# Optimization experiments

Measured on AMD Instinct MI355X. Metric: run time of the kernel, lower is better.

The kernel has to match this reference:

```python
import jax, jax.numpy as jnp
import numpy as np

B, LD, D, CONV = 2048, 100, 128, 128
C = CONV * 4  # 512
KS = (4, 6, 8)  # drug conv kernels -> Ld = 100 - 15 = 85


def setup_inputs() -> dict:
    key = jax.random.key(0)
    ks = jax.random.split(key, 32)
    def w(k, shape):
        return jax.random.normal(k, shape, jnp.float32) * 0.05
    emb = w(ks[0], (65, D)).at[0].set(0.0)  # padding_idx=0
    return dict(
        drug=jax.random.randint(ks[1], (B, LD), 0, 65, jnp.int32),
        feature=jax.random.normal(ks[2], (B, 7), jnp.float32),
        emb=emb,
        dw1=w(ks[3], (CONV, D, KS[0])), db1=w(ks[4], (CONV,)),
        dw2=w(ks[5], (CONV * 2, CONV, KS[1])), db2=w(ks[6], (CONV * 2,)),
        dw3=w(ks[7], (C, CONV * 2, KS[2])), db3=w(ks[8], (C,)),
        fw1=w(ks[9], (CONV, 7, 3)), fb1=w(ks[10], (CONV,)),
        fw2=w(ks[11], (CONV * 2, CONV, 3)), fb2=w(ks[12], (CONV * 2,)),
        fw3=w(ks[13], (C, CONV * 2, 3)), fb3=w(ks[14], (C,)),
        Wda=w(ks[15], (C, C)), bda=w(ks[16], (C,)),
        Wfa=w(ks[17], (C, C)), bfa=w(ks[18], (C,)),
        Watt=w(ks[19], (C, C)), batt=w(ks[20], (C,)),
        W1=w(ks[21], (1024, 2 * C)), b1=w(ks[22], (1024,)),
        W2=w(ks[23], (1024, 1024)), b2=w(ks[24], (1024,)),
        W3=w(ks[25], (512, 1024)), b3=w(ks[26], (512,)),
        Wo=w(ks[27], (1, 512)), bo=w(ks[28], (1,)),
    )


def _conv1d(x, w, b, pad):
    # x: [B, Cin, L], w: [Cout, Cin, K] (torch layout)
    y = jax.lax.conv_general_dilated(x, w, (1,), [(pad, pad)],
                                     dimension_numbers=('NCH', 'OIH', 'NCH'))
    return y + b[None, :, None]


def reference(drug, feature, emb, dw1, db1, dw2, db2, dw3, db3,
              fw1, fb1, fw2, fb2, fw3, fb3,
              Wda, bda, Wfa, bfa, Watt, batt,
              W1, b1, W2, b2, W3, b3, Wo, bo):
    relu = jax.nn.relu
    # Drug CNN stack (valid convs)
    x = emb[drug].transpose(0, 2, 1)                    # [B, D, 100]
    h = relu(_conv1d(x, dw1, db1, 0))
    h = relu(_conv1d(h, dw2, db2, 0))
    drugConv = relu(_conv1d(h, dw3, db3, 0))            # [B, C, 85]
    drug_att = jnp.einsum('bcl,dc->bld', drugConv, Wda) + bda   # [B, 85, C]
    # Feature CNN stack (same-padded convs on length-1 sequence)
    f = feature.reshape(feature.shape[0], 7, -1)        # [B, 7, 1]
    h = relu(_conv1d(f, fw1, fb1, 1))
    h = relu(_conv1d(h, fw2, fb2, 1))
    featureNN = relu(_conv1d(h, fw3, fb3, 1))           # [B, C, 1]
    feature_att = jnp.einsum('bcl,dc->bld', featureNN, Wfa) + bfa  # [B, 1, C]
    # Broadcast outer-sum cross attention
    s = relu(drug_att[:, :, None, :] + feature_att[:, None, :, :])  # [B,85,1,C]
    A = jnp.einsum('bqfc,dc->bqfd', s, Watt) + batt
    comp = jax.nn.sigmoid(jnp.mean(A, axis=2).transpose(0, 2, 1))   # [B,C,85]
    feat = jax.nn.sigmoid(jnp.mean(A, axis=1).transpose(0, 2, 1))   # [B,C,1]
    drugConv = drugConv * (0.5 + comp)
    featureNN = featureNN * (0.5 + feat)
    vd = jnp.max(drugConv, axis=2)                      # global max pool, kernel == Ld
    vf = featureNN[:, :, 0]                             # squeeze(2), Lf == 1
    pair = jnp.concatenate([vd, vf], axis=1)            # [B, 2C]
    leaky = lambda z: jnp.where(z > 0, z, 0.01 * z)
    h1 = leaky(pair @ W1.T + b1)
    h2 = leaky(h1 @ W2.T + b2)
    h3 = leaky(h2 @ W3.T + b3)
    return h3 @ Wo.T + bo                               # [B, 1]
```

## Files before the change

### kernel.cpp

```cpp
#include <hip/hip_runtime.h>
#include <cstdint>
#include <cstddef>

typedef unsigned short ushort_t;
typedef __bf16 bf16x8 __attribute__((ext_vector_type(8)));
typedef float floatx4 __attribute__((ext_vector_type(4)));

#define DEV static __device__ __forceinline__

DEV ushort_t f2bf(float f){
  union { float f; uint32_t u; } v; v.f = f;
  uint32_t u = v.u;
  return (ushort_t)((u + 0x7fffu + ((u >> 16) & 1u)) >> 16);
}
DEV float bf2f(ushort_t h){
  union { uint32_t u; float f; } v; v.u = ((uint32_t)h) << 16; return v.f;
}
DEV float sigmoidf_(float x){ return 1.f / (1.f + __expf(-x)); }

#define AS1 __attribute__((address_space(1)))
#define AS3 __attribute__((address_space(3)))
DEV void gld_lds16(const void* g, void* l){
  __builtin_amdgcn_global_load_lds((const AS1 void*)g, (AS3 void*)l, 16, 0, 0);
}

DEV void swz_xy(int& nx, int& my){
  int gx = gridDim.x, gy = gridDim.y;
  int lin = blockIdx.x + gx * blockIdx.y;
  int full = gy & ~7;
  int region = full * gx;
  if (lin < region){ int q = lin >> 3; nx = q % gx; my = (q / gx) * 8 + (lin & 7); }
  else { int r = lin - region; nx = r % gx; my = full + r / gx; }
}

#define BN 2048
#define LD 100
#define DIM 128
#define L1 97
#define L2 92
#define L3 85
#define CC 512

struct PrepArgs {
  const float *dw1,*dw2,*dw3,*Wda,*Wfa,*Watt,*W1,*W2,*W3,*fw1,*fw2,*fw3;
  ushort_t *bt1,*bt2,*bt3,*bWda,*bWfa,*bWatt,*bW1,*bW2,*bW3;
  float *fw1m,*fw2m,*fw3m;
};

__global__ void prep_k(PrepArgs a){
  int t0 = blockIdx.x * blockDim.x + threadIdx.x;
  int stride = gridDim.x * blockDim.x;
  switch (blockIdx.y){
  case 0:
    for (int i=t0;i<128*512;i+=stride){ int o=i>>9, rem=i&511, kk=rem>>7, c=rem&127;
      a.bt1[i]=f2bf(a.dw1[o*512 + c*4 + kk]); } break;
  case 1:
    for (int i=t0;i<256*768;i+=stride){ int o=i/768, rem=i-o*768, kk=rem>>7, c=rem&127;
      a.bt2[i]=f2bf(a.dw2[o*768 + c*6 + kk]); } break;
  case 2:
    for (int i=t0;i<512*2048;i+=stride){ int o=i>>11, rem=i&2047, kk=rem>>8, c=rem&255;
      a.bt3[i]=f2bf(a.dw3[o*2048 + c*8 + kk]); } break;
  case 3: for (int i=t0;i<262144;i+=stride) a.bWda[i]=f2bf(a.Wda[i]); break;
  case 4: for (int i=t0;i<262144;i+=stride) a.bWfa[i]=f2bf(a.Wfa[i]); break;
  case 5: for (int i=t0;i<262144;i+=stride) a.bWatt[i]=f2bf(a.Watt[i]); break;
  case 6: for (int i=t0;i<1048576;i+=stride) a.bW1[i]=f2bf(a.W1[i]); break;
  case 7: for (int i=t0;i<1048576;i+=stride) a.bW2[i]=f2bf(a.W2[i]); break;
  case 8: for (int i=t0;i<524288;i+=stride) a.bW3[i]=f2bf(a.W3[i]); break;
  case 9:  for (int i=t0;i<7*128;i+=stride){ int ii=i>>7, o=i&127; a.fw1m[i]=a.fw1[o*21 + ii*3 + 1]; } break;
  case 10: for (int i=t0;i<128*256;i+=stride){ int ii=i>>8, o=i&255; a.fw2m[i]=a.fw2[o*384 + ii*3 + 1]; } break;
  case 11: for (int i=t0;i<256*512;i+=stride){ int ii=i>>9, o=i&511; a.fw3m[i]=a.fw3[o*768 + ii*3 + 1]; } break;
  }
}

__global__ void gather_k(const int* __restrict__ drug, const float* __restrict__ emb,
                         ushort_t* __restrict__ x, int total){
  int g = blockIdx.x * blockDim.x + threadIdx.x;
  if (g >= total) return;
  int c8 = g & 15; int t = g >> 4;
  int tok = drug[t];
  const float* src = emb + (size_t)tok*DIM + c8*8;
  ushort_t* dst = x + ((size_t)t*DIM + c8*8);
  #pragma unroll
  for (int k=0;k<8;k++) dst[k] = f2bf(src[k]);
}

__global__ void featnn_k(const float* __restrict__ feature,
                         const float* __restrict__ fw1m, const float* __restrict__ fb1,
                         const float* __restrict__ fw2m, const float* __restrict__ fb2,
                         const float* __restrict__ fw3m, const float* __restrict__ fb3,
                         float* __restrict__ fnnf, ushort_t* __restrict__ fnnb)
{
  __shared__ float fs[8][7];
  __shared__ float h1s[8][128];
  __shared__ float h2s[8][256];
  int b0 = blockIdx.x * 8;
  int tid = threadIdx.x;
  if (tid < 56){ int bb = tid/7, i = tid - bb*7; fs[bb][i] = feature[(b0+bb)*7 + i]; }
  __syncthreads();
  if (tid < 128){
    float acc[8]; float bias = fb1[tid];
    #pragma unroll
    for (int bb=0;bb<8;bb++) acc[bb]=bias;
    for (int i=0;i<7;i++){ float wv = fw1m[i*128+tid];
      #pragma unroll
      for (int bb=0;bb<8;bb++) acc[bb] += wv*fs[bb][i]; }
    #pragma unroll
    for (int bb=0;bb<8;bb++) h1s[bb][tid]=fmaxf(acc[bb],0.f);
  }
  __syncthreads();
  {
    float acc[8]; float bias = fb2[tid];
    #pragma unroll
    for (int bb=0;bb<8;bb++) acc[bb]=bias;
    for (int i=0;i<128;i++){ float wv = fw2m[i*256+tid];
      #pragma unroll
      for (int bb=0;bb<8;bb++) acc[bb] += wv*h1s[bb][i]; }
    #pragma unroll
    for (int bb=0;bb<8;bb++) h2s[bb][tid]=fmaxf(acc[bb],0.f);
  }
  __syncthreads();
  #pragma unroll
  for (int oo=0;oo<2;oo++){
    int o = tid + oo*256;
    float acc[8]; float bias = fb3[o];
    #pragma unroll
    for (int bb=0;bb<8;bb++) acc[bb]=bias;
    for (int i=0;i<256;i++){ float wv = fw3m[i*512+o];
      #pragma unroll
      for (int bb=0;bb<8;bb++) acc[bb] += wv*h2s[bb][i]; }
    #pragma unroll
    for (int bb=0;bb<8;bb++){
      float v = fmaxf(acc[bb],0.f);
      fnnf[(size_t)(b0+bb)*CC + o] = v;
      fnnb[(size_t)(b0+bb)*CC + o] = f2bf(v);
    }
  }
}

enum { EP_RELU_BIAS=0, EP_RELU_BIAS_FATT=1, EP_ATT=2, EP_LEAKY_BIAS=3, EP_BIAS_F32=4 };

template<int EP>
__global__ __launch_bounds__(256,3) void gemm_k(
    const ushort_t* __restrict__ A, const ushort_t* __restrict__ Bt,
    int K, int LoutA, int LinA, int CinA,
    const float* __restrict__ bias, const float* __restrict__ fatt,
    void* __restrict__ outp, int ldo,
    const ushort_t* __restrict__ dcp, float* __restrict__ asum_g, float* __restrict__ tmax_g)
{
  __shared__ __align__(16) ushort_t As[128*64];
  __shared__ __align__(16) ushort_t Bs[128*64];
  const int tid  = threadIdx.x;
  const int lane = tid & 63;
  const int w    = tid >> 6;
  int nx, my; swz_xy(nx, my);
  const int m0 = my * 128;
  const int n0 = nx * 128;
  const int chunk = (lane & 7) ^ (lane >> 3);

  const ushort_t* pa[4];
  const ushort_t* pb[4];
  #pragma unroll
  for (int it=0; it<4; ++it){
    int row = it*32 + w*8 + (lane>>3);
    int r = m0 + row;
    int bb = r / LoutA;
    int ll = r - bb*LoutA;
    pa[it] = A  + ((size_t)(bb*LinA + ll) * (size_t)CinA + (size_t)chunk*8);
    pb[it] = Bt + ((size_t)(n0+row) * (size_t)K + (size_t)chunk*8);
  }

  floatx4 acc[4][4];
  #pragma unroll
  for (int i=0;i<4;i++)
    #pragma unroll
    for (int j=0;j<4;j++) acc[i][j] = (floatx4){0.f,0.f,0.f,0.f};

  const int mw = (w & 1) * 64;
  const int nw = (w >> 1) * 64;

  for (int k0=0; k0<K; k0+=64){
    #pragma unroll
    for (int it=0; it<4; ++it){
      gld_lds16(pa[it], &As[(it*32 + w*8)*64]);
      gld_lds16(pb[it], &Bs[(it*32 + w*8)*64]);
      pa[it] += 64; pb[it] += 64;
    }
    __syncthreads();
    #pragma unroll
    for (int ks=0; ks<2; ++ks){
      bf16x8 af[4], bfr[4];
      #pragma unroll
      for (int i=0;i<4;i++){
        int rowa = mw + i*16 + (lane & 15);
        int rowb = nw + i*16 + (lane & 15);
        int j = ks*4 + (lane >> 4);
        af[i]  = *(const bf16x8*)&As[rowa*64 + ((j ^ (rowa & 7)) << 3)];
        bfr[i] = *(const bf16x8*)&Bs[rowb*64 + ((j ^ (rowb & 7)) << 3)];
      }
      #pragma unroll
      for (int i=0;i<4;i++)
        #pragma unroll
        for (int j=0;j<4;j++)
          acc[i][j] = __builtin_amdgcn_mfma_f32_16x16x32_bf16(af[i], bfr[j], acc[i][j], 0, 0, 0);
    }
    __syncthreads();
  }

  if constexpr (EP == EP_ATT){
    __shared__ float red_sum[3*128];
    __shared__ int   red_max[3*128];
    const int bfirst = m0 / L3;
    for (int t2 = tid; t2 < 3*128; t2 += 256){ red_sum[t2] = 0.f; red_max[t2] = 0; }
    __syncthreads();
    const int segA = (m0 + mw) / L3 - bfirst;
    #pragma unroll
    for (int j=0;j<4;j++){
      int col = nw + j*16 + (lane & 15);
      int n = n0 + col;
      float bi = bias[n];
      float s0 = 0.f, s1 = 0.f, x0 = 0.f, x1 = 0.f;
      #pragma unroll
      for (int i=0;i<4;i++){
        #pragma unroll
        for (int r4=0;r4<4;r4++){
          int m = m0 + mw + i*16 + (lane>>4)*4 + r4;
          float Av = acc[i][j][r4] + bi;
          float dcv = bf2f(dcp[(size_t)m*CC + n]);
          float tv = dcv * (0.5f + sigmoidf_(Av));
          if ((m / L3 - bfirst) == segA){ s0 += Av; x0 = fmaxf(x0, tv); }
          else                          { s1 += Av; x1 = fmaxf(x1, tv); }
        }
      }
      atomicAdd(&red_sum[segA*128 + col], s0);
      atomicMax(&red_max[segA*128 + col], __float_as_int(x0));
      if (segA + 1 < 3){
        atomicAdd(&red_sum[(segA+1)*128 + col], s1);
        atomicMax(&red_max[(segA+1)*128 + col], __float_as_int(x1));
      }
    }
    __syncthreads();
    for (int t2 = tid; t2 < 3*128; t2 += 256){
      int seg = t2 >> 7, col = t2 & 127;
      int b = bfirst + seg;
      if (b * L3 < m0 + 128){
        atomicAdd(asum_g + (size_t)b*CC + n0 + col, red_sum[t2]);
        atomicMax((int*)tmax_g + (size_t)b*CC + n0 + col, red_max[t2]);
      }
    }
    return;
  }

  float* outf = (float*)outp;
  ushort_t* outh = (ushort_t*)outp;
  #pragma unroll
  for (int i=0;i<4;i++){
    #pragma unroll
    for (int j=0;j<4;j++){
      #pragma unroll
      for (int r4=0;r4<4;r4++){
        int m = m0 + mw + i*16 + (lane>>4)*4 + r4;
        int n = n0 + nw + j*16 + (lane & 15);
        float v = acc[i][j][r4] + bias[n];
        if constexpr (EP == EP_RELU_BIAS)       v = fmaxf(v, 0.f);
        else if constexpr (EP == EP_RELU_BIAS_FATT){ v += fatt[(m / L3)*CC + n]; v = fmaxf(v, 0.f); }
        else if constexpr (EP == EP_LEAKY_BIAS) v = v > 0.f ? v : 0.01f*v;
        if constexpr (EP == EP_BIAS_F32) outf[(size_t)m*ldo + n] = v;
        else                             outh[(size_t)m*ldo + n] = f2bf(v);
      }
    }
  }
}

__global__ void reduce2_k(const float* __restrict__ asum, const float* __restrict__ tmax,
                          const float* __restrict__ fnnf, ushort_t* __restrict__ pair)
{
  int g = blockIdx.x * blockDim.x + threadIdx.x;
  if (g >= BN * CC) return;
  int b = g >> 9, c = g & 511;
  pair[(size_t)b*1024 + c] = f2bf(tmax[g]);
  float fv = fnnf[g] * (0.5f + sigmoidf_(asum[g] * (1.f/(float)L3)));
  pair[(size_t)b*1024 + 512 + c] = f2bf(fv);
}

__global__ void final_k(const ushort_t* __restrict__ h3, const float* __restrict__ Wo,
                        const float* __restrict__ bo, float* __restrict__ out)
{
  int b = blockIdx.x*4 + (threadIdx.x >> 6);
  int lane = threadIdx.x & 63;
  float acc = 0.f;
  for (int i=lane; i<512; i+=64) acc += bf2f(h3[(size_t)b*512 + i]) * Wo[i];
  #pragma unroll
  for (int off=32; off; off>>=1) acc += __shfl_down(acc, off);
  if (lane == 0) out[b] = acc + bo[0];
}

extern "C" void kernel_launch(void* const* d_in, const int* in_sizes, int n_in,
                              void* d_out, int out_size, void* d_ws, size_t ws_size,
                              hipStream_t stream)
{
  (void)in_sizes; (void)n_in; (void)out_size;
  const int*   drug    = (const int*)  d_in[0];
  const float* feature = (const float*)d_in[1];
  const float* emb     = (const float*)d_in[2];
  const float* dw1 = (const float*)d_in[3];  const float* db1 = (const float*)d_in[4];
  const float* dw2 = (const float*)d_in[5];  const float* db2 = (const float*)d_in[6];
  const float* dw3 = (const float*)d_in[7];  const float* db3 = (const float*)d_in[8];
  const float* fw1 = (const float*)d_in[9];  const float* fb1 = (const float*)d_in[10];
  const float* fw2 = (const float*)d_in[11]; const float* fb2 = (const float*)d_in[12];
  const float* fw3 = (const float*)d_in[13]; const float* fb3 = (const float*)d_in[14];
  const float* Wda = (const float*)d_in[15]; const float* bda = (const float*)d_in[16];
  const float* Wfa = (const float*)d_in[17]; const float* bfa = (const float*)d_in[18];
  const float* Watt= (const float*)d_in[19]; const float* batt= (const float*)d_in[20];
  const float* W1  = (const float*)d_in[21]; const float* b1  = (const float*)d_in[22];
  const float* W2  = (const float*)d_in[23]; const float* b2  = (const float*)d_in[24];
  const float* W3  = (const float*)d_in[25]; const float* b3  = (const float*)d_in[26];
  const float* Wo  = (const float*)d_in[27]; const float* bo  = (const float*)d_in[28];
  float* out = (float*)d_out;

  size_t off = 0; char* base = (char*)d_ws;
  auto alloc = [&](size_t bytes)->char*{
    off = (off + 255) & ~(size_t)255; char* p = base + off; off += bytes; return p;
  };
  ushort_t* bt1  = (ushort_t*)alloc(128*512*2);
  ushort_t* bt2  = (ushort_t*)alloc(256*768*2);
  ushort_t* bt3  = (ushort_t*)alloc((size_t)512*2048*2);
  ushort_t* bWda = (ushort_t*)alloc(262144*2);
  ushort_t* bWfa = (ushort_t*)alloc(262144*2);
  ushort_t* bWatt= (ushort_t*)alloc(262144*2);
  ushort_t* bW1  = (ushort_t*)alloc((size_t)1048576*2);
  ushort_t* bW2  = (ushort_t*)alloc((size_t)1048576*2);
  ushort_t* bW3  = (ushort_t*)alloc((size_t)524288*2);
  float* fw1m = (float*)alloc(7*128*4);
  float* fw2m = (float*)alloc(128*256*4);
  float* fw3m = (float*)alloc(256*512*4);
  float* fnnf = (float*)alloc((size_t)BN*CC*4);
  ushort_t* fnnb = (ushort_t*)alloc((size_t)BN*CC*2);
  float* fattf = (float*)alloc((size_t)BN*CC*4);
  float* asum_g = (float*)alloc((size_t)BN*CC*4);
  float* tmax_g = (float*)alloc((size_t)BN*CC*4);
  ushort_t* pairb = (ushort_t*)alloc((size_t)BN*1024*2);
  ushort_t* m1b = (ushort_t*)alloc((size_t)BN*1024*2);
  ushort_t* m2b = (ushort_t*)alloc((size_t)BN*1024*2);
  ushort_t* m3b = (ushort_t*)alloc((size_t)BN*512*2);

  const size_t PER_SLABP = 97536, PER_DC = 87040, PER_CHUNK = 271616;
  size_t avail = (ws_size > off + 4096) ? (ws_size - off - 4096) : 0;
  int CH = (int)(avail / PER_CHUNK);
  if (CH > BN) CH = BN;
  CH = (CH / 128) * 128;
  if (CH < 128) CH = 128;
  char* chunkbase = alloc((size_t)CH*PER_CHUNK);
  ushort_t* xembC = (ushort_t*)chunkbase;
  ushort_t* h1C   = (ushort_t*)(chunkbase + (size_t)CH*25600);
  ushort_t* h2C   = (ushort_t*)(chunkbase + (size_t)CH*(25600+24832));
  ushort_t* dcC   = (ushort_t*)(chunkbase + (size_t)CH*PER_SLABP);
  ushort_t* sC    = (ushort_t*)(chunkbase + (size_t)CH*(PER_SLABP + PER_DC));

  PrepArgs pa;
  pa.dw1=dw1; pa.dw2=dw2; pa.dw3=dw3; pa.Wda=Wda; pa.Wfa=Wfa; pa.Watt=Watt;
  pa.W1=W1; pa.W2=W2; pa.W3=W3; pa.fw1=fw1; pa.fw2=fw2; pa.fw3=fw3;
  pa.bt1=bt1; pa.bt2=bt2; pa.bt3=bt3; pa.bWda=bWda; pa.bWfa=bWfa; pa.bWatt=bWatt;
  pa.bW1=bW1; pa.bW2=bW2; pa.bW3=bW3; pa.fw1m=fw1m; pa.fw2m=fw2m; pa.fw3m=fw3m;

  hipMemsetAsync(asum_g, 0, (size_t)BN*CC*4, stream);
  hipMemsetAsync(tmax_g, 0, (size_t)BN*CC*4, stream);
  prep_k<<<dim3(64,12), 256, 0, stream>>>(pa);
  featnn_k<<<BN/8, 256, 0, stream>>>(feature, fw1m, fb1, fw2m, fb2, fw3m, fb3, fnnf, fnnb);
  gemm_k<EP_BIAS_F32><<<dim3(4,16), 256, 0, stream>>>(fnnb, bWfa, 512, 1,1,512, bfa, nullptr, fattf, 512, nullptr,nullptr,nullptr);

  for (int b0c = 0; b0c < BN; b0c += CH){
    const int c = (BN - b0c < CH) ? (BN - b0c) : CH;
    const int t = c / 128;
    gather_k<<<(c*LD*(DIM/8) + 255)/256, 256, 0, stream>>>(drug + (size_t)b0c*LD, emb, xembC, c*LD*(DIM/8));
    gemm_k<EP_RELU_BIAS><<<dim3(1, t*L1), 256, 0, stream>>>(xembC, bt1, 512,  L1, LD, DIM, db1, nullptr, h1C, 128, nullptr,nullptr,nullptr);
    gemm_k<EP_RELU_BIAS><<<dim3(2, t*L2), 256, 0, stream>>>(h1C,  bt2, 768,  L2, L1, 128, db2, nullptr, h2C, 256, nullptr,nullptr,nullptr);
    gemm_k<EP_RELU_BIAS><<<dim3(4, t*L3), 256, 0, stream>>>(h2C,  bt3, 2048, L3, L2, 256, db3, nullptr, dcC,  512, nullptr,nullptr,nullptr);
    gemm_k<EP_RELU_BIAS_FATT><<<dim3(4, t*L3), 256, 0, stream>>>(dcC, bWda, 512, 1,1,512, bda, fattf + (size_t)b0c*CC, sC, 512, nullptr,nullptr,nullptr);
    gemm_k<EP_ATT><<<dim3(4, t*L3), 256, 0, stream>>>(sC, bWatt, 512, 1,1,512, batt, nullptr, nullptr, 512,
                                                      dcC, asum_g + (size_t)b0c*CC, tmax_g + (size_t)b0c*CC);
  }

  reduce2_k<<<(BN*CC + 255)/256, 256, 0, stream>>>(asum_g, tmax_g, fnnf, pairb);

  gemm_k<EP_LEAKY_BIAS><<<dim3(8,16), 256, 0, stream>>>(pairb, bW1, 1024, 1,1,1024, b1, nullptr, m1b, 1024, nullptr,nullptr,nullptr);
  gemm_k<EP_LEAKY_BIAS><<<dim3(8,16), 256, 0, stream>>>(m1b,  bW2, 1024, 1,1,1024, b2, nullptr, m2b, 1024, nullptr,nullptr,nullptr);
  gemm_k<EP_LEAKY_BIAS><<<dim3(4,16), 256, 0, stream>>>(m2b,  bW3, 1024, 1,1,1024, b3, nullptr, m3b, 512, nullptr,nullptr,nullptr);
  final_k<<<BN/4, 256, 0, stream>>>(m3b, Wo, bo, out);
}
```

Before: 1.079 ms.

## Fuse drug-attention and attention GEMMs into one kernel keeping s in LDS

Replaces the two back-to-back GEMMs (drugConv@Wda with fatt/ReLU, then s@Watt with the sigmoid/mean/max epilogue) with a single att_k kernel. Each block handles 64 rows, computes s in two 256-column halves directly into swizzled LDS, and accumulates the second GEMM's output in registers across both halves. This removes the global write and read-back of the s intermediate and one launch, and shrinks the per-chunk workspace so larger chunks fit. In exchange the kernel holds many more accumulator registers (launch bounds 2), uses 64-row tiles with repeated Wda/Watt reloads per block, and has no software pipelining, which may lower MFMA efficiency.

```diff
diff --git a/kernel.cpp b/kernel.cpp
--- a/kernel.cpp
+++ b/kernel.cpp
@@ -137,15 +137,14 @@
   }
 }
 
-enum { EP_RELU_BIAS=0, EP_RELU_BIAS_FATT=1, EP_ATT=2, EP_LEAKY_BIAS=3, EP_BIAS_F32=4 };
+enum { EP_RELU_BIAS=0, EP_RELU_BIAS_FATT=1, EP_LEAKY_BIAS=3, EP_BIAS_F32=4 };
 
 template<int EP>
 __global__ __launch_bounds__(256,3) void gemm_k(
     const ushort_t* __restrict__ A, const ushort_t* __restrict__ Bt,
     int K, int LoutA, int LinA, int CinA,
     const float* __restrict__ bias, const float* __restrict__ fatt,
-    void* __restrict__ outp, int ldo,
-    const ushort_t* __restrict__ dcp, float* __restrict__ asum_g, float* __restrict__ tmax_g)
+    void* __restrict__ outp, int ldo)
 {
   __shared__ __align__(16) ushort_t As[128*64];
   __shared__ __align__(16) ushort_t Bs[128*64];
@@ -206,50 +205,6 @@
     __syncthreads();
   }
 
-  if constexpr (EP == EP_ATT){
-    __shared__ float red_sum[3*128];
-    __shared__ int   red_max[3*128];
-    const int bfirst = m0 / L3;
-    for (int t2 = tid; t2 < 3*128; t2 += 256){ red_sum[t2] = 0.f; red_max[t2] = 0; }
-    __syncthreads();
-    const int segA = (m0 + mw) / L3 - bfirst;
-    #pragma unroll
-    for (int j=0;j<4;j++){
-      int col = nw + j*16 + (lane & 15);
-      int n = n0 + col;
-      float bi = bias[n];
-      float s0 = 0.f, s1 = 0.f, x0 = 0.f, x1 = 0.f;
-      #pragma unroll
-      for (int i=0;i<4;i++){
-        #pragma unroll
-        for (int r4=0;r4<4;r4++){
-          int m = m0 + mw + i*16 + (lane>>4)*4 + r4;
-          float Av = acc[i][j][r4] + bi;
-          float dcv = bf2f(dcp[(size_t)m*CC + n]);
-          float tv = dcv * (0.5f + sigmoidf_(Av));
-          if ((m / L3 - bfirst) == segA){ s0 += Av; x0 = fmaxf(x0, tv); }
-          else                          { s1 += Av; x1 = fmaxf(x1, tv); }
-        }
-      }
-      atomicAdd(&red_sum[segA*128 + col], s0);
-      atomicMax(&red_max[segA*128 + col], __float_as_int(x0));
-      if (segA + 1 < 3){
-        atomicAdd(&red_sum[(segA+1)*128 + col], s1);
-        atomicMax(&red_max[(segA+1)*128 + col], __float_as_int(x1));
-      }
-    }
-    __syncthreads();
-    for (int t2 = tid; t2 < 3*128; t2 += 256){
-      int seg = t2 >> 7, col = t2 & 127;
-      int b = bfirst + seg;
-      if (b * L3 < m0 + 128){
-        atomicAdd(asum_g + (size_t)b*CC + n0 + col, red_sum[t2]);
-        atomicMax((int*)tmax_g + (size_t)b*CC + n0 + col, red_max[t2]);
-      }
-    }
-    return;
-  }
-
   float* outf = (float*)outp;
   ushort_t* outh = (ushort_t*)outp;
   #pragma unroll
@@ -267,6 +222,180 @@
         if constexpr (EP == EP_BIAS_F32) outf[(size_t)m*ldo + n] = v;
         else                             outh[(size_t)m*ldo + n] = f2bf(v);
       }
+    }
+  }
+}
+
+__global__ __launch_bounds__(256,2) void att_k(
+    const ushort_t* __restrict__ dcp,
+    const ushort_t* __restrict__ bWda,
+    const float* __restrict__ bda,
+    const float* __restrict__ fatt,
+    const ushort_t* __restrict__ bWatt,
+    const float* __restrict__ batt,
+    float* __restrict__ asum_g, float* __restrict__ tmax_g)
+{
+  __shared__ __align__(16) ushort_t Sh[64*256];
+  __shared__ __align__(16) ushort_t Bs[128*64];
+  __shared__ __align__(16) ushort_t AsR[64*64];
+  float* red_sum = (float*)AsR;
+  int*   red_max = (int*)AsR + 1024;
+
+  const int tid  = threadIdx.x;
+  const int lane = tid & 63;
+  const int w    = tid >> 6;
+  const int m0   = blockIdx.x * 64;
+  const int mh   = (w & 1) * 32;
+  const int nh   = (w >> 1) * 64;
+  const int chunkb = (lane & 7) ^ (lane >> 3);
+
+  const ushort_t* paBase[2];
+  #pragma unroll
+  for (int it=0; it<2; ++it)
+    paBase[it] = dcp + (size_t)(m0 + it*32 + w*8 + (lane>>3))*CC + (size_t)chunkb*8;
+
+  floatx4 acc2[4][2][4];
+  #pragma unroll
+  for (int a=0;a<4;a++)
+    #pragma unroll
+    for (int i=0;i<2;i++)
+      #pragma unroll
+      for (int j=0;j<4;j++) acc2[a][i][j] = (floatx4){0.f,0.f,0.f,0.f};
+
+  for (int h=0; h<2; ++h){
+    #pragma unroll
+    for (int nt=0; nt<2; ++nt){
+      floatx4 acc[2][4];
+      #pragma unroll
+      for (int i=0;i<2;i++)
+        #pragma unroll
+        for (int j=0;j<4;j++) acc[i][j] = (floatx4){0.f,0.f,0.f,0.f};
+      const ushort_t* pa[2] = { paBase[0], paBase[1] };
+      const ushort_t* pb[4];
+      #pragma unroll
+      for (int it=0; it<4; ++it)
+        pb[it] = bWda + (size_t)(h*256 + nt*128 + it*32 + w*8 + (lane>>3))*CC + (size_t)chunkb*8;
+
+      for (int k0=0; k0<512; k0+=64){
+        #pragma unroll
+        for (int it=0; it<2; ++it){ gld_lds16(pa[it], &AsR[(it*32 + w*8)*64]); pa[it] += 64; }
+        #pragma unroll
+        for (int it=0; it<4; ++it){ gld_lds16(pb[it], &Bs[(it*32 + w*8)*64]);  pb[it] += 64; }
+        __syncthreads();
+        #pragma unroll
+        for (int ks=0; ks<2; ++ks){
+          bf16x8 af[2], bfr[4];
+          int j = ks*4 + (lane >> 4);
+          #pragma unroll
+          for (int i=0;i<2;i++){
+            int rowa = mh + i*16 + (lane & 15);
+            af[i] = *(const bf16x8*)&AsR[rowa*64 + ((j ^ (rowa & 7)) << 3)];
+          }
+          #pragma unroll
+          for (int j2=0;j2<4;j2++){
+            int rowb = nh + j2*16 + (lane & 15);
+            bfr[j2] = *(const bf16x8*)&Bs[rowb*64 + ((j ^ (rowb & 7)) << 3)];
+          }
+          #pragma unroll
+          for (int i=0;i<2;i++)
+            #pragma unroll
+            for (int j2=0;j2<4;j2++)
+              acc[i][j2] = __builtin_amdgcn_mfma_f32_16x16x32_bf16(af[i], bfr[j2], acc[i][j2], 0, 0, 0);
+        }
+        __syncthreads();
+      }
+      #pragma unroll
+      for (int i=0;i<2;i++){
+        #pragma unroll
+        for (int j2=0;j2<4;j2++){
+          #pragma unroll
+          for (int r4=0;r4<4;r4++){
+            int row = mh + i*16 + (lane>>4)*4 + r4;
+            int cl  = nt*128 + nh + j2*16 + (lane & 15);
+            int gn  = h*256 + cl;
+            float v = acc[i][j2][r4] + bda[gn] + fatt[(size_t)((m0+row)/L3)*CC + gn];
+            v = fmaxf(v, 0.f);
+            Sh[row*256 + ((((cl>>3) ^ (row & 7)) << 3) | (cl & 7))] = f2bf(v);
+          }
+        }
+      }
+    }
+    __syncthreads();
+
+    #pragma unroll
+    for (int nt2=0; nt2<4; ++nt2){
+      const ushort_t* pb[4];
+      #pragma unroll
+      for (int it=0; it<4; ++it)
+        pb[it] = bWatt + (size_t)(nt2*128 + it*32 + w*8 + (lane>>3))*CC + h*256 + (size_t)chunkb*8;
+      for (int k0=0; k0<256; k0+=64){
+        #pragma unroll
+        for (int it=0; it<4; ++it){ gld_lds16(pb[it], &Bs[(it*32 + w*8)*64]); pb[it] += 64; }
+        __syncthreads();
+        #pragma unroll
+        for (int ks=0; ks<2; ++ks){
+          bf16x8 af[2], bfr[4];
+          int j = ks*4 + (lane >> 4);
+          int cj = (k0 >> 3) + j;
+          #pragma unroll
+          for (int i=0;i<2;i++){
+            int row = mh + i*16 + (lane & 15);
+            af[i] = *(const bf16x8*)&Sh[row*256 + ((cj ^ (row & 7)) << 3)];
+          }
+          #pragma unroll
+          for (int j2=0;j2<4;j2++){
+            int rowb = nh + j2*16 + (lane & 15);
+            bfr[j2] = *(const bf16x8*)&Bs[rowb*64 + ((j ^ (rowb & 7)) << 3)];
+          }
+          #pragma unroll
+          for (int i=0;i<2;i++)
+            #pragma unroll
+            for (int j2=0;j2<4;j2++)
+              acc2[nt2][i][j2] = __builtin_amdgcn_mfma_f32_16x16x32_bf16(af[i], bfr[j2], acc2[nt2][i][j2], 0, 0, 0);
+        }
+        __syncthreads();
+      }
+    }
+  }
+
+  for (int t2 = tid; t2 < 1024; t2 += 256){ red_sum[t2] = 0.f; red_max[t2] = 0; }
+  __syncthreads();
+  const int bfirst = m0 / L3;
+  const int segW = (m0 + mh) / L3 - bfirst;
+  #pragma unroll
+  for (int nt2=0; nt2<4; ++nt2){
+    #pragma unroll
+    for (int j2=0;j2<4;j2++){
+      int n = nt2*128 + nh + j2*16 + (lane & 15);
+      float s0=0.f, s1=0.f, x0=0.f, x1=0.f;
+      float bi = batt[n];
+      #pragma unroll
+      for (int i=0;i<2;i++){
+        #pragma unroll
+        for (int r4=0;r4<4;r4++){
+          int m = m0 + mh + i*16 + (lane>>4)*4 + r4;
+          float Av = acc2[nt2][i][j2][r4] + bi;
+          float dcv = bf2f(dcp[(size_t)m*CC + n]);
+          float tv = dcv * (0.5f + sigmoidf_(Av));
+          if (m / L3 - bfirst == segW){ s0 += Av; x0 = fmaxf(x0, tv); }
+          else                        { s1 += Av; x1 = fmaxf(x1, tv); }
+        }
+      }
+      atomicAdd(&red_sum[segW*512 + n], s0);
+      atomicMax(&red_max[segW*512 + n], __float_as_int(x0));
+      if (segW == 0){
+        atomicAdd(&red_sum[512 + n], s1);
+        atomicMax(&red_max[512 + n], __float_as_int(x1));
+      }
+    }
+  }
+  __syncthreads();
+  for (int t2 = tid; t2 < 1024; t2 += 256){
+    int seg = t2 >> 9, col = t2 & 511;
+    int b = bfirst + seg;
+    if (b*L3 < m0 + 64 && b*L3 + L3 > m0){
+      atomicAdd(asum_g + (size_t)b*CC + col, red_sum[t2]);
+      atomicMax((int*)tmax_g + (size_t)b*CC + col, red_max[t2]);
     }
   }
 }
@@ -343,7 +472,7 @@
   ushort_t* m2b = (ushort_t*)alloc((size_t)BN*1024*2);
   ushort_t* m3b = (ushort_t*)alloc((size_t)BN*512*2);
 
-  const size_t PER_SLABP = 97536, PER_DC = 87040, PER_CHUNK = 271616;
+  const size_t PER_SLABP = 97536, PER_DC = 87040, PER_CHUNK = PER_SLABP + PER_DC;
   size_t avail = (ws_size > off + 4096) ? (ws_size - off - 4096) : 0;
   int CH = (int)(avail / PER_CHUNK);
   if (CH > BN) CH = BN;
@@ -354,7 +483,6 @@
   ushort_t* h1C   = (ushort_t*)(chunkbase + (size_t)CH*25600);
   ushort_t* h2C   = (ushort_t*)(chunkbase + (size_t)CH*(25600+24832));
   ushort_t* dcC   = (ushort_t*)(chunkbase + (size_t)CH*PER_SLABP);
-  ushort_t* sC    = (ushort_t*)(chunkbase + (size_t)CH*(PER_SLABP + PER_DC));
 
   PrepArgs pa;
   pa.dw1=dw1; pa.dw2=dw2; pa.dw3=dw3; pa.Wda=Wda; pa.Wfa=Wfa; pa.Watt=Watt;
@@ -366,24 +494,23 @@
   hipMemsetAsync(tmax_g, 0, (size_t)BN*CC*4, stream);
   prep_k<<<dim3(64,12), 256, 0, stream>>>(pa);
   featnn_k<<<BN/8, 256, 0, stream>>>(feature, fw1m, fb1, fw2m, fb2, fw3m, fb3, fnnf, fnnb);
-  gemm_k<EP_BIAS_F32><<<dim3(4,16), 256, 0, stream>>>(fnnb, bWfa, 512, 1,1,512, bfa, nullptr, fattf, 512, nullptr,nullptr,nullptr);
+  gemm_k<EP_BIAS_F32><<<dim3(4,16), 256, 0, stream>>>(fnnb, bWfa, 512, 1,1,512, bfa, nullptr, fattf, 512);
 
   for (int b0c = 0; b0c < BN; b0c += CH){
     const int c = (BN - b0c < CH) ? (BN - b0c) : CH;
     const int t = c / 128;
     gather_k<<<(c*LD*(DIM/8) + 255)/256, 256, 0, stream>>>(drug + (size_t)b0c*LD, emb, xembC, c*LD*(DIM/8));
-    gemm_k<EP_RELU_BIAS><<<dim3(1, t*L1), 256, 0, stream>>>(xembC, bt1, 512,  L1, LD, DIM, db1, nullptr, h1C, 128, nullptr,nullptr,nullptr);
-    gemm_k<EP_RELU_BIAS><<<dim3(2, t*L2), 256, 0, stream>>>(h1C,  bt2, 768,  L2, L1, 128, db2, nullptr, h2C, 256, nullptr,nullptr,nullptr);
-    gemm_k<EP_RELU_BIAS><<<dim3(4, t*L3), 256, 0, stream>>>(h2C,  bt3, 2048, L3, L2, 256, db3, nullptr, dcC,  512, nullptr,nullptr,nullptr);
-    gemm_k<EP_RELU_BIAS_FATT><<<dim3(4, t*L3), 256, 0, stream>>>(dcC, bWda, 512, 1,1,512, bda, fattf + (size_t)b0c*CC, sC, 512, nullptr,nullptr,nullptr);
-    gemm_k<EP_ATT><<<dim3(4, t*L3), 256, 0, stream>>>(sC, bWatt, 512, 1,1,512, batt, nullptr, nullptr, 512,
-                                                      dcC, asum_g + (size_t)b0c*CC, tmax_g + (size_t)b0c*CC);
+    gemm_k<EP_RELU_BIAS><<<dim3(1, t*L1), 256, 0, stream>>>(xembC, bt1, 512,  L1, LD, DIM, db1, nullptr, h1C, 128);
+    gemm_k<EP_RELU_BIAS><<<dim3(2, t*L2), 256, 0, stream>>>(h1C,  bt2, 768,  L2, L1, 128, db2, nullptr, h2C, 256);
+    gemm_k<EP_RELU_BIAS><<<dim3(4, t*L3), 256, 0, stream>>>(h2C,  bt3, 2048, L3, L2, 256, db3, nullptr, dcC,  512);
+    att_k<<<dim3(t*170), 256, 0, stream>>>(dcC, bWda, bda, fattf + (size_t)b0c*CC, bWatt, batt,
+                                           asum_g + (size_t)b0c*CC, tmax_g + (size_t)b0c*CC);
   }
 
   reduce2_k<<<(BN*CC + 255)/256, 256, 0, stream>>>(asum_g, tmax_g, fnnf, pairb);
 
-  gemm_k<EP_LEAKY_BIAS><<<dim3(8,16), 256, 0, stream>>>(pairb, bW1, 1024, 1,1,1024, b1, nullptr, m1b, 1024, nullptr,nullptr,nullptr);
-  gemm_k<EP_LEAKY_BIAS><<<dim3(8,16), 256, 0, stream>>>(m1b,  bW2, 1024, 1,1,1024, b2, nullptr, m2b, 1024, nullptr,nullptr,nullptr);
-  gemm_k<EP_LEAKY_BIAS><<<dim3(4,16), 256, 0, stream>>>(m2b,  bW3, 1024, 1,1,1024, b3, nullptr, m3b, 512, nullptr,nullptr,nullptr);
+  gemm_k<EP_LEAKY_BIAS><<<dim3(8,16), 256, 0, stream>>>(pairb, bW1, 1024, 1,1,1024, b1, nullptr, m1b, 1024);
+  gemm_k<EP_LEAKY_BIAS><<<dim3(8,16), 256, 0, stream>>>(m1b,  bW2, 1024, 1,1,1024, b2, nullptr, m2b, 1024);
+  gemm_k<EP_LEAKY_BIAS><<<dim3(4,16), 256, 0, stream>>>(m2b,  bW3, 1024, 1,1,1024, b3, nullptr, m3b, 512);
   final_k<<<BN/4, 256, 0, stream>>>(m3b, Wo, bo, out);
 }
```

New measurement: 1.607 ms. +48.8%, slower.

## Fuse embedding gather into first drug conv GEMM and ping-pong chunk buffers

Applied to the files above, without the earlier changes.

Replaces the separate gather kernel plus first conv GEMM with a single kernel that converts the 65-row embedding table to bf16 in LDS and reads A fragments directly by token index. This removes the materialized embedding activation buffer and one launch. Intermediate buffers are reduced to two ping-pong slabs, which allows larger batch chunks for the same workspace. Each block redundantly converts the whole embedding table, and the A-side LDS reads are unswizzled token lookups that may cause bank conflicts.

```diff
diff --git a/kernel.cpp b/kernel.cpp
--- a/kernel.cpp
+++ b/kernel.cpp
@@ -72,18 +72,6 @@
   }
 }
 
-__global__ void gather_k(const int* __restrict__ drug, const float* __restrict__ emb,
-                         ushort_t* __restrict__ x, int total){
-  int g = blockIdx.x * blockDim.x + threadIdx.x;
-  if (g >= total) return;
-  int c8 = g & 15; int t = g >> 4;
-  int tok = drug[t];
-  const float* src = emb + (size_t)tok*DIM + c8*8;
-  ushort_t* dst = x + ((size_t)t*DIM + c8*8);
-  #pragma unroll
-  for (int k=0;k<8;k++) dst[k] = f2bf(src[k]);
-}
-
 __global__ void featnn_k(const float* __restrict__ feature,
                          const float* __restrict__ fw1m, const float* __restrict__ fb1,
                          const float* __restrict__ fw2m, const float* __restrict__ fb2,
@@ -133,6 +121,92 @@
       float v = fmaxf(acc[bb],0.f);
       fnnf[(size_t)(b0+bb)*CC + o] = v;
       fnnb[(size_t)(b0+bb)*CC + o] = f2bf(v);
+    }
+  }
+}
+
+__global__ __launch_bounds__(256,3) void conv1_k(
+    const int* __restrict__ drug,
+    const float* __restrict__ emb,
+    const ushort_t* __restrict__ bt1,
+    const float* __restrict__ db1,
+    ushort_t* __restrict__ h1)
+{
+  __shared__ __align__(16) ushort_t Bs[128*64];
+  __shared__ __align__(16) ushort_t Emb[65*136];
+  __shared__ uint8_t Tok[128*4];
+  const int tid  = threadIdx.x;
+  const int lane = tid & 63;
+  const int w    = tid >> 6;
+  const int m0   = blockIdx.x * 128;
+
+  for (int idx = tid; idx < 65*128; idx += 256){
+    int t2 = idx >> 7, c = idx & 127;
+    Emb[t2*136 + c] = f2bf(emb[idx]);
+  }
+  for (int idx = tid; idx < 128*4; idx += 256){
+    int row = idx >> 2, kk = idx & 3;
+    int r = m0 + row;
+    int b = r / L1, l = r - b*L1;
+    Tok[idx] = (uint8_t)drug[b*LD + l + kk];
+  }
+
+  const int chunk = (lane & 7) ^ (lane >> 3);
+  const ushort_t* pb[4];
+  #pragma unroll
+  for (int it=0; it<4; ++it)
+    pb[it] = bt1 + (size_t)(it*32 + w*8 + (lane>>3))*512 + (size_t)chunk*8;
+
+  floatx4 acc[4][4];
+  #pragma unroll
+  for (int i=0;i<4;i++)
+    #pragma unroll
+    for (int j=0;j<4;j++) acc[i][j] = (floatx4){0.f,0.f,0.f,0.f};
+
+  const int mw = (w & 1) * 64;
+  const int nw = (w >> 1) * 64;
+
+  for (int k0=0; k0<512; k0+=64){
+    #pragma unroll
+    for (int it=0; it<4; ++it){ gld_lds16(pb[it], &Bs[(it*32 + w*8)*64]); pb[it] += 64; }
+    __syncthreads();
+    #pragma unroll
+    for (int ks=0; ks<2; ++ks){
+      int j  = ks*4 + (lane >> 4);
+      int kg = k0 + j*8;
+      int kk = kg >> 7, c0 = kg & 127;
+      bf16x8 af[4], bfr[4];
+      #pragma unroll
+      for (int i=0;i<4;i++){
+        int rowa = mw + i*16 + (lane & 15);
+        int tok = Tok[rowa*4 + kk];
+        af[i] = *(const bf16x8*)&Emb[tok*136 + c0];
+      }
+      #pragma unroll
+      for (int j2=0;j2<4;j2++){
+        int rowb = nw + j2*16 + (lane & 15);
+        bfr[j2] = *(const bf16x8*)&Bs[rowb*64 + ((j ^ (rowb & 7)) << 3)];
+      }
+      #pragma unroll
+      for (int i=0;i<4;i++)
+        #pragma unroll
+        for (int j2=0;j2<4;j2++)
+          acc[i][j2] = __builtin_amdgcn_mfma_f32_16x16x32_bf16(af[i], bfr[j2], acc[i][j2], 0, 0, 0);
+    }
+    __syncthreads();
+  }
+
+  #pragma unroll
+  for (int i=0;i<4;i++){
+    #pragma unroll
+    for (int j2=0;j2<4;j2++){
+      #pragma unroll
+      for (int r4=0;r4<4;r4++){
+        int r = m0 + mw + i*16 + (lane>>4)*4 + r4;
+        int n = nw + j2*16 + (lane & 15);
+        float v = fmaxf(acc[i][j2][r4] + db1[n], 0.f);
+        h1[(size_t)r*128 + n] = f2bf(v);
+      }
     }
   }
 }
@@ -343,18 +417,15 @@
   ushort_t* m2b = (ushort_t*)alloc((size_t)BN*1024*2);
   ushort_t* m3b = (ushort_t*)alloc((size_t)BN*512*2);
 
-  const size_t PER_SLABP = 97536, PER_DC = 87040, PER_CHUNK = 271616;
+  const size_t PER_BUF = 87040, PER_CHUNK = 2*PER_BUF;
   size_t avail = (ws_size > off + 4096) ? (ws_size - off - 4096) : 0;
   int CH = (int)(avail / PER_CHUNK);
   if (CH > BN) CH = BN;
   CH = (CH / 128) * 128;
   if (CH < 128) CH = 128;
   char* chunkbase = alloc((size_t)CH*PER_CHUNK);
-  ushort_t* xembC = (ushort_t*)chunkbase;
-  ushort_t* h1C   = (ushort_t*)(chunkbase + (size_t)CH*25600);
-  ushort_t* h2C   = (ushort_t*)(chunkbase + (size_t)CH*(25600+24832));
-  ushort_t* dcC   = (ushort_t*)(chunkbase + (size_t)CH*PER_SLABP);
-  ushort_t* sC    = (ushort_t*)(chunkbase + (size_t)CH*(PER_SLABP + PER_DC));
+  ushort_t* bufA = (ushort_t*)chunkbase;
+  ushort_t* bufB = (ushort_t*)(chunkbase + (size_t)CH*PER_BUF);
 
   PrepArgs pa;
   pa.dw1=dw1; pa.dw2=dw2; pa.dw3=dw3; pa.Wda=Wda; pa.Wfa=Wfa; pa.Watt=Watt;
@@ -371,13 +442,12 @@
   for (int b0c = 0; b0c < BN; b0c += CH){
     const int c = (BN - b0c < CH) ? (BN - b0c) : CH;
     const int t = c / 128;
-    gather_k<<<(c*LD*(DIM/8) + 255)/256, 256, 0, stream>>>(drug + (size_t)b0c*LD, emb, xembC, c*LD*(DIM/8));
-    gemm_k<EP_RELU_BIAS><<<dim3(1, t*L1), 256, 0, stream>>>(xembC, bt1, 512,  L1, LD, DIM, db1, nullptr, h1C, 128, nullptr,nullptr,nullptr);
-    gemm_k<EP_RELU_BIAS><<<dim3(2, t*L2), 256, 0, stream>>>(h1C,  bt2, 768,  L2, L1, 128, db2, nullptr, h2C, 256, nullptr,nullptr,nullptr);
-    gemm_k<EP_RELU_BIAS><<<dim3(4, t*L3), 256, 0, stream>>>(h2C,  bt3, 2048, L3, L2, 256, db3, nullptr, dcC,  512, nullptr,nullptr,nullptr);
-    gemm_k<EP_RELU_BIAS_FATT><<<dim3(4, t*L3), 256, 0, stream>>>(dcC, bWda, 512, 1,1,512, bda, fattf + (size_t)b0c*CC, sC, 512, nullptr,nullptr,nullptr);
-    gemm_k<EP_ATT><<<dim3(4, t*L3), 256, 0, stream>>>(sC, bWatt, 512, 1,1,512, batt, nullptr, nullptr, 512,
-                                                      dcC, asum_g + (size_t)b0c*CC, tmax_g + (size_t)b0c*CC);
+    conv1_k<<<dim3(t*L1), 256, 0, stream>>>(drug + (size_t)b0c*LD, emb, bt1, db1, bufB);
+    gemm_k<EP_RELU_BIAS><<<dim3(2, t*L2), 256, 0, stream>>>(bufB, bt2, 768,  L2, L1, 128, db2, nullptr, bufA, 256, nullptr,nullptr,nullptr);
+    gemm_k<EP_RELU_BIAS><<<dim3(4, t*L3), 256, 0, stream>>>(bufA, bt3, 2048, L3, L2, 256, db3, nullptr, bufB, 512, nullptr,nullptr,nullptr);
+    gemm_k<EP_RELU_BIAS_FATT><<<dim3(4, t*L3), 256, 0, stream>>>(bufB, bWda, 512, 1,1,512, bda, fattf + (size_t)b0c*CC, bufA, 512, nullptr,nullptr,nullptr);
+    gemm_k<EP_ATT><<<dim3(4, t*L3), 256, 0, stream>>>(bufA, bWatt, 512, 1,1,512, batt, nullptr, nullptr, 512,
+                                                      bufB, asum_g + (size_t)b0c*CC, tmax_g + (size_t)b0c*CC);
   }
 
   reduce2_k<<<(BN*CC + 255)/256, 256, 0, stream>>>(asum_g, tmax_g, fnnf, pairb);
```

Result: no change. 1.071 ms (-0.8%).
